# Performance work log

Measured on AMD Instinct MI355X. Metric: run time of the kernel, lower is better.

## Reference

```python
import jax, jax.numpy as jnp
import numpy as np

NEG_SLOPE = 0.2  # PyG GATConv default LeakyReLU slope


def _gat(h, src, dst, num_nodes, W, a_src, a_dst, bias):
    """PyG-style GATConv (concat=True, eval mode, self-loops already in src/dst)."""
    heads, out = a_src.shape
    hp = (h @ W).reshape(num_nodes, heads, out)          # (N, H, F)
    e_s = (hp * a_src).sum(-1)                            # (N, H)
    e_d = (hp * a_dst).sum(-1)                            # (N, H)
    e = jax.nn.leaky_relu(e_s[src] + e_d[dst], NEG_SLOPE)  # (E, H)
    m = jax.ops.segment_max(e, dst, num_segments=num_nodes)
    w = jnp.exp(e - m[dst])
    z = jax.ops.segment_sum(w, dst, num_segments=num_nodes)
    alpha = w / (z[dst] + 1e-16)                          # softmax over in-edges per dst
    agg = jax.ops.segment_sum(hp[src] * alpha[:, :, None], dst, num_segments=num_nodes)
    return agg.reshape(num_nodes, heads * out) + bias


def setup_inputs() -> dict:
    key = jax.random.key(0)
    ks = jax.random.split(key, 20)
    N, T, Fin, H, heads, E = 30000, 4, 256, 64, 4, 240000
    D = H * heads  # 256
    s = 0.05
    p = lambda k, shape: (jax.random.normal(k, shape, jnp.float32) * s)
    return {
        "x": jax.random.normal(ks[0], (N, T, Fin), jnp.float32),
        "edge_index": jax.random.randint(ks[1], (2, E), 0, N, jnp.int32),
        "Wp": p(ks[2], (Fin, H)), "bp": p(ks[3], (H,)),
        "W0": p(ks[4], (H, D)), "a_src0": p(ks[5], (heads, H)), "a_dst0": p(ks[6], (heads, H)), "b0": p(ks[7], (D,)),
        "W1": p(ks[8], (D, D)), "a_src1": p(ks[9], (heads, H)), "a_dst1": p(ks[10], (heads, H)), "b1": p(ks[11], (D,)),
        "Wq": p(ks[12], (D, D)), "bq": p(ks[13], (D,)),
        "Wk": p(ks[14], (D, D)), "bk": p(ks[15], (D,)),
        "Wv": p(ks[16], (D, D)), "bv": p(ks[17], (D,)),
    }


def reference(x, edge_index, Wp, bp, W0, a_src0, a_dst0, b0, W1, a_src1, a_dst1, b1,
              Wq, bq, Wk, bk, Wv, bv):
    N, T, Fin = x.shape
    D = Wq.shape[0]
    loops = jnp.arange(N, dtype=edge_index.dtype)
    src = jnp.concatenate([edge_index[0], loops])  # add self-loops (PyG default)
    dst = jnp.concatenate([edge_index[1], loops])
    xT = jnp.transpose(x, (1, 0, 2))  # (T, N, Fin)

    def step(_, xt):
        h = xt @ Wp + bp
        h = jax.nn.elu(_gat(h, src, dst, N, W0, a_src0, a_dst0, b0))
        h = jax.nn.elu(_gat(h, src, dst, N, W1, a_src1, a_dst1, b1))
        return None, h

    _, embs = jax.lax.scan(step, None, xT)  # (T, N, D)

    # temporal attention
    Q = embs @ Wq + bq
    K = embs @ Wk + bk
    V = embs @ Wv + bv
    Q_time = Q.mean(axis=1)  # (T, D)
    K_time = K.mean(axis=1)  # (T, D)
    scores = (Q_time @ K_time.T) / jnp.sqrt(jnp.asarray(D, jnp.float32))
    attn = jax.nn.softmax(scores, axis=1)            # (T, T)
    Vr = V.reshape(T, -1)                            # (T, N*D)
    attended = attn @ Vr                             # (T, N*D)
    return attended[-1].reshape(N, D)
```

## Files before the change

### kernel.cpp

```cpp
#include <hip/hip_runtime.h>
#include <math.h>

#define NEG_SLOPE 0.2f

typedef __attribute__((ext_vector_type(8))) short short8;
typedef __attribute__((ext_vector_type(4))) float f32x4;

__device__ inline unsigned short f2bf(float f){
  union { float f; unsigned u; } v; v.f = f;
  unsigned r = v.u + 0x7fffu + ((v.u >> 16) & 1u);
  return (unsigned short)(r >> 16);
}
__device__ inline float bf2f(unsigned u){
  union { unsigned u; float f; } v; v.u = u << 16; return v.f;
}

__global__ __launch_bounds__(256) void k_deg_count(const int* __restrict__ dst, int E, int* __restrict__ deg){
  int i = blockIdx.x*256 + threadIdx.x;
  if (i < E) atomicAdd(&deg[dst[i]], 1);
}
__global__ __launch_bounds__(256) void k_scan_blk(const int* __restrict__ deg, int* __restrict__ rowptr,
                                                  int* __restrict__ bsum, int N){
  __shared__ int ws[4];
  int tid = threadIdx.x;
  int i = blockIdx.x*256 + tid;
  int v = (i < N) ? deg[i]+1 : 0;
  int lane = tid & 63, w = tid >> 6;
  int s = v;
  #pragma unroll
  for (int off=1; off<64; off<<=1){
    int u = __shfl_up(s, off);
    if (lane >= off) s += u;
  }
  if (lane == 63) ws[w] = s;
  __syncthreads();
  int woff = 0;
  #pragma unroll
  for (int k=0;k<4;k++) if (k < w) woff += ws[k];
  int incl = s + woff;
  if (i < N) rowptr[i] = incl - v;
  if (tid == 255) bsum[blockIdx.x] = incl;
}
__global__ __launch_bounds__(256) void k_scan_top(int* __restrict__ bsum, int nb, int* __restrict__ rowptrN){
  __shared__ int buf[256];
  int tid = threadIdx.x;
  int v = (tid < nb) ? bsum[tid] : 0;
  buf[tid] = v;
  __syncthreads();
  for (int off=1; off<256; off<<=1){
    int add = (tid >= off) ? buf[tid-off] : 0;
    __syncthreads();
    buf[tid] += add;
    __syncthreads();
  }
  if (tid < nb) bsum[tid] = buf[tid] - v;
  if (tid == 0) rowptrN[0] = buf[255];
}
__global__ __launch_bounds__(256) void k_scan_fix(int* __restrict__ rowptr, const int* __restrict__ bsum,
                                                  int* __restrict__ pos, int* __restrict__ colidx, int N){
  int i = blockIdx.x*256 + threadIdx.x;
  if (i < N){
    int r = rowptr[i] + bsum[blockIdx.x];
    rowptr[i] = r;
    colidx[r] = i;
    pos[i] = r + 1;
  }
}
__global__ __launch_bounds__(256) void k_fill_edges(const int* __restrict__ src, const int* __restrict__ dst,
                                                    int E, int* __restrict__ pos, int* __restrict__ colidx){
  int i = blockIdx.x*256 + threadIdx.x;
  if (i < E){
    int d = dst[i];
    colidx[atomicAdd(&pos[d],1)] = src[i];
  }
}

__global__ __launch_bounds__(256) void k_prep(const float* __restrict__ Wp, const float* __restrict__ W0,
                                              const float* __restrict__ W1, const float* __restrict__ Wv,
                                              const float* __restrict__ as0, const float* __restrict__ ad0,
                                              unsigned short* __restrict__ WpT, unsigned short* __restrict__ W0T4,
                                              unsigned short* __restrict__ W1T, unsigned short* __restrict__ WvT,
                                              float* __restrict__ ahs, float* __restrict__ ahd,
                                              int* __restrict__ deg, float* __restrict__ sume, int N){
  int idx = blockIdx.x*256 + threadIdx.x;
  if (idx < 16384){
    int k = idx >> 6, p = idx & 63;
    WpT[p*256 + k] = f2bf(Wp[idx]);
  } else if (idx < 32768){
    int i = idx - 16384;
    int h = i >> 12, r = i & 4095, p = r >> 6, k = r & 63;
    W0T4[i] = f2bf(W0[k*256 + h*64 + p]);
  } else if (idx < 98304){
    int i = idx - 32768; int k = i >> 8, p = i & 255;
    W1T[p*256 + k] = f2bf(W1[i]);
  } else if (idx < 163840){
    int i = idx - 98304; int k = i >> 8, p = i & 255;
    WvT[p*256 + k] = f2bf(Wv[i]);
  } else if (idx < 164096){
    int i = idx - 163840;
    int h = i >> 6, d = i & 63;
    float ss = 0.f, sd = 0.f;
    for (int j=0;j<64;j++){
      float w = W0[d*256 + h*64 + j];
      ss += w * as0[h*64 + j];
      sd += w * ad0[h*64 + j];
    }
    ahs[i] = ss; ahd[i] = sd;
  } else if (idx < 165120){
    sume[idx - 164096] = 0.f;
  } else if (idx < 165120 + N){
    deg[idx - 165120] = 0;
  }
}

__global__ __launch_bounds__(256) void k_h0(const float* __restrict__ A,
                                            const unsigned short* __restrict__ Bt,
                                            const float* __restrict__ bias,
                                            unsigned short* __restrict__ C, int M, int Nn){
  int wid = blockIdx.x*4 + (threadIdx.x >> 6);
  int m0 = wid * 64;
  if (m0 >= M) return;
  int lane = threadIdx.x & 63;
  int lr = lane & 15, g = lane >> 4, lk = g*8;
  const float* Arow[4];
  #pragma unroll
  for (int m=0;m<4;m++){
    int row = m0 + m*16 + lr;
    if (row > M-1) row = M-1;
    Arow[m] = A + (size_t)row*256 + lk;
  }
  const unsigned short* Bb = Bt + (size_t)lr*256 + lk;
  f32x4 acc[4][4];
  #pragma unroll
  for (int m=0;m<4;m++)
    #pragma unroll
    for (int n=0;n<4;n++)
      #pragma unroll
      for (int j=0;j<4;j++) acc[m][n][j] = 0.f;

  #pragma unroll 2
  for (int ks=0; ks<8; ks++){
    int k0 = ks*32;
    short8 bfr[4];
    #pragma unroll
    for (int n=0;n<4;n++)
      bfr[n] = *(const short8*)(Bb + (size_t)n*16*256 + k0);
    short8 afr[4];
    #pragma unroll
    for (int m=0;m<4;m++){
      float4 u = *(const float4*)(Arow[m] + k0);
      float4 w = *(const float4*)(Arow[m] + k0 + 4);
      afr[m][0]=(short)f2bf(u.x); afr[m][1]=(short)f2bf(u.y);
      afr[m][2]=(short)f2bf(u.z); afr[m][3]=(short)f2bf(u.w);
      afr[m][4]=(short)f2bf(w.x); afr[m][5]=(short)f2bf(w.y);
      afr[m][6]=(short)f2bf(w.z); afr[m][7]=(short)f2bf(w.w);
    }
    #pragma unroll
    for (int m=0;m<4;m++)
      #pragma unroll
      for (int n=0;n<4;n++)
        acc[m][n] = __builtin_amdgcn_mfma_f32_16x16x32_bf16(afr[m], bfr[n], acc[m][n], 0,0,0);
  }
  #pragma unroll
  for (int n=0;n<4;n++){
    int col = n*16 + lr;
    float bcol = bias[col];
    #pragma unroll
    for (int m=0;m<4;m++){
      #pragma unroll
      for (int j=0;j<4;j++){
        int row = m0 + m*16 + g*4 + j;
        if (row < M){
          int t = row & 3, nn = row >> 2;
          C[(size_t)t*Nn*64 + (size_t)nn*64 + col] = f2bf(acc[m][n][j] + bcol);
        }
      }
    }
  }
}

__global__ __launch_bounds__(256) void k_gat01(const unsigned short* __restrict__ A,
                                               const unsigned short* __restrict__ W0T4,
                                               const float* __restrict__ b0,
                                               const unsigned short* __restrict__ W1T,
                                               const float* __restrict__ as1,
                                               const float* __restrict__ ad1,
                                               unsigned short* __restrict__ hp,
                                               float* __restrict__ e_s, float* __restrict__ e_d,
                                               int M){
  __shared__ unsigned short H1[64][264];
  __shared__ unsigned short Bls[128][72];
  int tid = threadIdx.x;
  int m0 = blockIdx.x * 64;
  int wave = tid >> 6, lane = tid & 63;
  int lr = lane & 15, g4 = lane >> 4, lk = g4*8;
  int rbase = m0 + wave*16;

  {
    f32x4 acc1[16];
    #pragma unroll
    for (int q=0;q<16;q++)
      #pragma unroll
      for (int j=0;j<4;j++) acc1[q][j] = 0.f;
    int arow = rbase + lr; if (arow > M-1) arow = M-1;
    #pragma unroll
    for (int h=0;h<4;h++){
      short8 afr[2];
      #pragma unroll
      for (int ks=0;ks<2;ks++)
        afr[ks] = *(const short8*)(A + (size_t)arow*256 + h*64 + ks*32 + lk);
      #pragma unroll
      for (int nn=0;nn<4;nn++){
        #pragma unroll
        for (int ks=0;ks<2;ks++){
          short8 bfr = *(const short8*)(W0T4 + ((size_t)h*64 + nn*16 + lr)*64 + ks*32 + lk);
          acc1[h*4+nn] = __builtin_amdgcn_mfma_f32_16x16x32_bf16(afr[ks], bfr, acc1[h*4+nn], 0,0,0);
        }
      }
    }
    #pragma unroll
    for (int q=0;q<16;q++){
      int col = q*16 + lr;
      float bcol = b0[col];
      #pragma unroll
      for (int j=0;j<4;j++){
        float v = acc1[q][j] + bcol;
        v = (v > 0.f) ? v : (__expf(v) - 1.f);
        H1[wave*16 + g4*4 + j][col] = f2bf(v);
      }
    }
  }
  __syncthreads();

  float esp0[4], esp1[4], esp2[4], esp3[4];
  float edp0[4], edp1[4], edp2[4], edp3[4];
  #pragma unroll
  for (int j=0;j<4;j++){ esp0[j]=0.f; esp1[j]=0.f; esp2[j]=0.f; esp3[j]=0.f;
                         edp0[j]=0.f; edp1[j]=0.f; edp2[j]=0.f; edp3[j]=0.f; }

  #pragma unroll
  for (int chalf=0; chalf<2; chalf++){
    f32x4 acc2[8];
    #pragma unroll
    for (int q=0;q<8;q++)
      #pragma unroll
      for (int j=0;j<4;j++) acc2[q][j] = 0.f;
    for (int k0=0;k0<256;k0+=64){
      #pragma unroll
      for (int it=0; it<4; it++){
        int idx = tid + it*256;
        int p = idx >> 3, ch = (idx & 7)*8;
        *(uint4*)(&Bls[p][ch]) = *(const uint4*)(W1T + (size_t)(chalf*128 + p)*256 + k0 + ch);
      }
      __syncthreads();
      #pragma unroll
      for (int ks=0;ks<2;ks++){
        short8 afr = *(const short8*)(&H1[wave*16 + lr][k0 + ks*32 + lk]);
        #pragma unroll
        for (int q=0;q<8;q++){
          short8 bfr = *(const short8*)(&Bls[q*16 + lr][ks*32 + lk]);
          acc2[q] = __builtin_amdgcn_mfma_f32_16x16x32_bf16(afr, bfr, acc2[q], 0,0,0);
        }
      }
      __syncthreads();
    }
    #pragma unroll
    for (int q=0;q<8;q++){
      int col = chalf*128 + q*16 + lr;
      float asv = as1[col], adv = ad1[col];
      #pragma unroll
      for (int j=0;j<4;j++){
        int row = m0 + wave*16 + g4*4 + j;
        float v = acc2[q][j];
        if (row < M)
          hp[(size_t)row*256 + col] = f2bf(v);
        if (chalf==0 && (q>>2)==0){ esp0[j] += v*asv; edp0[j] += v*adv; }
        if (chalf==0 && (q>>2)==1){ esp1[j] += v*asv; edp1[j] += v*adv; }
        if (chalf==1 && (q>>2)==0){ esp2[j] += v*asv; edp2[j] += v*adv; }
        if (chalf==1 && (q>>2)==1){ esp3[j] += v*asv; edp3[j] += v*adv; }
      }
    }
  }

  #pragma unroll
  for (int j=0;j<4;j++){
    #pragma unroll
    for (int off=1; off<16; off<<=1){
      esp0[j] += __shfl_xor(esp0[j], off); edp0[j] += __shfl_xor(edp0[j], off);
      esp1[j] += __shfl_xor(esp1[j], off); edp1[j] += __shfl_xor(edp1[j], off);
      esp2[j] += __shfl_xor(esp2[j], off); edp2[j] += __shfl_xor(edp2[j], off);
      esp3[j] += __shfl_xor(esp3[j], off); edp3[j] += __shfl_xor(edp3[j], off);
    }
  }
  if (lr < 4){
    #pragma unroll
    for (int j=0;j<4;j++){
      int row = m0 + wave*16 + g4*4 + j;
      if (row < M){
        float ev = (lr==0)?esp0[j]:((lr==1)?esp1[j]:((lr==2)?esp2[j]:esp3[j]));
        float dv = (lr==0)?edp0[j]:((lr==1)?edp1[j]:((lr==2)?edp2[j]:edp3[j]));
        e_s[(size_t)row*4 + lr] = ev;
        e_d[(size_t)row*4 + lr] = dv;
      }
    }
  }
}

__global__ __launch_bounds__(512) void k_gemm_fin(const unsigned short* __restrict__ embs,
                                                  const float* __restrict__ awp,
                                                  const unsigned short* __restrict__ Bt,
                                                  const float* __restrict__ bias,
                                                  float* __restrict__ C, int M){
  constexpr int K = 256, BK = 64, PAD = 8;
  __shared__ unsigned short Als[128][BK+PAD];
  __shared__ unsigned short Bls[256][BK+PAD];
  int tid = threadIdx.x;
  int m0  = blockIdx.x * 128;
  int wave = tid >> 6, lane = tid & 63;
  int wr = wave & 3, wc = wave >> 2;
  int lr = lane & 15, lk = (lane >> 4) * 8;
  float a0=awp[0], a1=awp[1], a2=awp[2], a3=awp[3];
  size_t sl = (size_t)M*256;
  f32x4 acc[2][8];
  #pragma unroll
  for (int m=0;m<2;m++)
    #pragma unroll
    for (int n=0;n<8;n++)
      #pragma unroll
      for (int j=0;j<4;j++) acc[m][n][j] = 0.f;

  for (int k0 = 0; k0 < K; k0 += BK){
    #pragma unroll
    for (int i=0;i<2;i++){
      int idx = tid + i*512;
      int r = idx >> 3, ch = (idx & 7)*8;
      int row = m0 + r;
      uint4 w = make_uint4(0,0,0,0);
      if (row < M){
        size_t o = (size_t)row*256 + k0 + ch;
        uint4 u0 = *(const uint4*)(embs + o);
        uint4 u1 = *(const uint4*)(embs + o + sl);
        uint4 u2 = *(const uint4*)(embs + o + 2*sl);
        uint4 u3 = *(const uint4*)(embs + o + 3*sl);
        const unsigned* p0=&u0.x; const unsigned* p1=&u1.x;
        const unsigned* p2=&u2.x; const unsigned* p3=&u3.x;
        unsigned* pw=&w.x;
        #pragma unroll
        for (int q=0;q<4;q++){
          float lo = a0*bf2f(p0[q]&0xffffu) + a1*bf2f(p1[q]&0xffffu) + a2*bf2f(p2[q]&0xffffu) + a3*bf2f(p3[q]&0xffffu);
          float hi = a0*bf2f(p0[q]>>16)     + a1*bf2f(p1[q]>>16)     + a2*bf2f(p2[q]>>16)     + a3*bf2f(p3[q]>>16);
          pw[q] = (unsigned)f2bf(lo) | ((unsigned)f2bf(hi) << 16);
        }
      }
      *(uint4*)(&Als[r][ch]) = w;
    }
    #pragma unroll
    for (int i=0;i<4;i++){
      int idx = tid + i*512;
      int r = idx >> 3, ch = (idx & 7)*8;
      *(uint4*)(&Bls[r][ch]) = *(const uint4*)(Bt + (size_t)r*K + k0 + ch);
    }
    __syncthreads();
    #pragma unroll
    for (int ks=0; ks<2; ks++){
      short8 afr[2], bfr[8];
      #pragma unroll
      for (int m=0;m<2;m++)
        afr[m] = *(const short8*)(&Als[wr*32 + m*16 + lr][ks*32 + lk]);
      #pragma unroll
      for (int n=0;n<8;n++)
        bfr[n] = *(const short8*)(&Bls[wc*128 + n*16 + lr][ks*32 + lk]);
      #pragma unroll
      for (int m=0;m<2;m++)
        #pragma unroll
        for (int n=0;n<8;n++)
          acc[m][n] = __builtin_amdgcn_mfma_f32_16x16x32_bf16(afr[m], bfr[n], acc[m][n], 0,0,0);
    }
    __syncthreads();
  }
  #pragma unroll
  for (int m=0;m<2;m++){
    #pragma unroll
    for (int n=0;n<8;n++){
      int col = wc*128 + n*16 + lr;
      float bcol = bias[col];
      #pragma unroll
      for (int j=0;j<4;j++){
        int row = m0 + wr*32 + m*16 + (lane>>4)*4 + j;
        if (row < M)
          C[(size_t)row*256 + col] = acc[m][n][j] + bcol;
      }
    }
  }
}

__global__ __launch_bounds__(256) void k_esd0(const unsigned short* __restrict__ h0,
                                              const float* __restrict__ ahs, const float* __restrict__ ahd,
                                              float* __restrict__ e_s, float* __restrict__ e_d, int M){
  int n = blockIdx.x*4 + (threadIdx.x >> 6);
  if (n >= M) return;
  int lane = threadIdx.x & 63;
  int h = lane >> 4, l4 = (lane & 15)*4;
  uint2 v = *(const uint2*)(h0 + (size_t)n*64 + l4);
  float v0 = bf2f(v.x & 0xffffu), v1 = bf2f(v.x >> 16);
  float v2 = bf2f(v.y & 0xffffu), v3 = bf2f(v.y >> 16);
  float4 as = *(const float4*)(ahs + h*64 + l4);
  float4 ad = *(const float4*)(ahd + h*64 + l4);
  float ps = v0*as.x + v1*as.y + v2*as.z + v3*as.w;
  float pd = v0*ad.x + v1*ad.y + v2*ad.z + v3*ad.w;
  #pragma unroll
  for (int off=1; off<16; off<<=1){ ps += __shfl_xor(ps,off); pd += __shfl_xor(pd,off); }
  if ((lane & 15) == 0){
    e_s[n*4+h] = ps; e_d[n*4+h] = pd;
  }
}

__global__ __launch_bounds__(256) void k_agg0(const unsigned short* __restrict__ h0all,
                                              const float* __restrict__ e_s, const float* __restrict__ e_d,
                                              const int* __restrict__ rowptr, const int* __restrict__ colidx,
                                              unsigned short* __restrict__ agg, int N){
  int n = blockIdx.x*4 + (threadIdx.x >> 6);
  if (n >= N) return;
  int t = blockIdx.y;
  int g = t*N + n;
  int lane = threadIdx.x & 63;
  int half = lane >> 5, l = lane & 31;
  int h = l >> 3, di = (l & 7)*8;
  int s0 = rowptr[n], s1 = rowptr[n+1];
  float ed = e_d[(size_t)g*4 + h];
  const unsigned short* h0t = h0all + (size_t)t*N*64;
  const float* est = e_s + (size_t)t*N*4;
  float z = 0.f;
  float a[8] = {0,0,0,0,0,0,0,0};
  int i = s0;
  for (; i+6 <= s1; i += 6){
    int sA = colidx[i + half];
    int sB = colidx[i + 2 + half];
    int sC = colidx[i + 4 + half];
    uint4 vA = *(const uint4*)(h0t + (size_t)sA*64 + di);
    uint4 vB = *(const uint4*)(h0t + (size_t)sB*64 + di);
    uint4 vC = *(const uint4*)(h0t + (size_t)sC*64 + di);
    float eA = est[sA*4 + h] + ed;
    float eB = est[sB*4 + h] + ed;
    float eC = est[sC*4 + h] + ed;
    eA = fmaxf(eA, NEG_SLOPE*eA); eB = fmaxf(eB, NEG_SLOPE*eB); eC = fmaxf(eC, NEG_SLOPE*eC);
    float wA = __expf(eA), wB = __expf(eB), wC = __expf(eC);
    z += wA + wB + wC;
    a[0] += wA*bf2f(vA.x&0xffffu) + wB*bf2f(vB.x&0xffffu) + wC*bf2f(vC.x&0xffffu);
    a[1] += wA*bf2f(vA.x>>16)     + wB*bf2f(vB.x>>16)     + wC*bf2f(vC.x>>16);
    a[2] += wA*bf2f(vA.y&0xffffu) + wB*bf2f(vB.y&0xffffu) + wC*bf2f(vC.y&0xffffu);
    a[3] += wA*bf2f(vA.y>>16)     + wB*bf2f(vB.y>>16)     + wC*bf2f(vC.y>>16);
    a[4] += wA*bf2f(vA.z&0xffffu) + wB*bf2f(vB.z&0xffffu) + wC*bf2f(vC.z&0xffffu);
    a[5] += wA*bf2f(vA.z>>16)     + wB*bf2f(vB.z>>16)     + wC*bf2f(vC.z>>16);
    a[6] += wA*bf2f(vA.w&0xffffu) + wB*bf2f(vB.w&0xffffu) + wC*bf2f(vC.w&0xffffu);
    a[7] += wA*bf2f(vA.w>>16)     + wB*bf2f(vB.w>>16)     + wC*bf2f(vC.w>>16);
  }
  for (; i+2 <= s1; i += 2){
    int s = colidx[i + half];
    uint4 v = *(const uint4*)(h0t + (size_t)s*64 + di);
    float e = est[s*4 + h] + ed;
    e = fmaxf(e, NEG_SLOPE*e);
    float w = __expf(e);
    z += w;
    a[0] += w*bf2f(v.x&0xffffu); a[1] += w*bf2f(v.x>>16);
    a[2] += w*bf2f(v.y&0xffffu); a[3] += w*bf2f(v.y>>16);
    a[4] += w*bf2f(v.z&0xffffu); a[5] += w*bf2f(v.z>>16);
    a[6] += w*bf2f(v.w&0xffffu); a[7] += w*bf2f(v.w>>16);
  }
  if (i < s1 && half == 0){
    int s = colidx[i];
    uint4 v = *(const uint4*)(h0t + (size_t)s*64 + di);
    float e = est[s*4 + h] + ed;
    e = fmaxf(e, NEG_SLOPE*e);
    float w = __expf(e);
    z += w;
    a[0] += w*bf2f(v.x&0xffffu); a[1] += w*bf2f(v.x>>16);
    a[2] += w*bf2f(v.y&0xffffu); a[3] += w*bf2f(v.y>>16);
    a[4] += w*bf2f(v.z&0xffffu); a[5] += w*bf2f(v.z>>16);
    a[6] += w*bf2f(v.w&0xffffu); a[7] += w*bf2f(v.w>>16);
  }
  z += __shfl_xor(z, 32);
  #pragma unroll
  for (int q=0;q<8;q++) a[q] += __shfl_xor(a[q], 32);
  if (half == 0){
    float inv = 1.f / (z + 1e-16f);
    uint4 r;
    r.x = (unsigned)f2bf(a[0]*inv) | ((unsigned)f2bf(a[1]*inv) << 16);
    r.y = (unsigned)f2bf(a[2]*inv) | ((unsigned)f2bf(a[3]*inv) << 16);
    r.z = (unsigned)f2bf(a[4]*inv) | ((unsigned)f2bf(a[5]*inv) << 16);
    r.w = (unsigned)f2bf(a[6]*inv) | ((unsigned)f2bf(a[7]*inv) << 16);
    *(uint4*)(agg + (size_t)g*256 + l*8) = r;
  }
}

__global__ __launch_bounds__(256) void k_agg(const unsigned short* __restrict__ hpall,
                                             const float* __restrict__ e_s, const float* __restrict__ e_d,
                                             const int* __restrict__ rowptr, const int* __restrict__ colidx,
                                             const float* __restrict__ bias, unsigned short* __restrict__ outb,
                                             int N){
  int n = blockIdx.x*4 + (threadIdx.x >> 6);
  if (n >= N) return;
  int t = blockIdx.y;
  int g = t*N + n;
  int lane = threadIdx.x & 63;
  int half = lane >> 5, l = lane & 31;
  int h = l >> 3, d0 = l*8;
  int s0 = rowptr[n], s1 = rowptr[n+1];
  float ed = e_d[(size_t)g*4 + h];
  const unsigned short* hpt = hpall + (size_t)t*N*256;
  const float* est = e_s + (size_t)t*N*4;
  float z = 0.f;
  float a[8] = {0,0,0,0,0,0,0,0};
  int i = s0;
  for (; i+6 <= s1; i += 6){
    int sA = colidx[i + half];
    int sB = colidx[i + 2 + half];
    int sC = colidx[i + 4 + half];
    uint4 vA = *(const uint4*)(hpt + (size_t)sA*256 + d0);
    uint4 vB = *(const uint4*)(hpt + (size_t)sB*256 + d0);
    uint4 vC = *(const uint4*)(hpt + (size_t)sC*256 + d0);
    float eA = est[sA*4 + h] + ed;
    float eB = est[sB*4 + h] + ed;
    float eC = est[sC*4 + h] + ed;
    eA = fmaxf(eA, NEG_SLOPE*eA); eB = fmaxf(eB, NEG_SLOPE*eB); eC = fmaxf(eC, NEG_SLOPE*eC);
    float wA = __expf(eA), wB = __expf(eB), wC = __expf(eC);
    z += wA + wB + wC;
    a[0] += wA*bf2f(vA.x&0xffffu) + wB*bf2f(vB.x&0xffffu) + wC*bf2f(vC.x&0xffffu);
    a[1] += wA*bf2f(vA.x>>16)     + wB*bf2f(vB.x>>16)     + wC*bf2f(vC.x>>16);
    a[2] += wA*bf2f(vA.y&0xffffu) + wB*bf2f(vB.y&0xffffu) + wC*bf2f(vC.y&0xffffu);
    a[3] += wA*bf2f(vA.y>>16)     + wB*bf2f(vB.y>>16)     + wC*bf2f(vC.y>>16);
    a[4] += wA*bf2f(vA.z&0xffffu) + wB*bf2f(vB.z&0xffffu) + wC*bf2f(vC.z&0xffffu);
    a[5] += wA*bf2f(vA.z>>16)     + wB*bf2f(vB.z>>16)     + wC*bf2f(vC.z>>16);
    a[6] += wA*bf2f(vA.w&0xffffu) + wB*bf2f(vB.w&0xffffu) + wC*bf2f(vC.w&0xffffu);
    a[7] += wA*bf2f(vA.w>>16)     + wB*bf2f(vB.w>>16)     + wC*bf2f(vC.w>>16);
  }
  for (; i+2 <= s1; i += 2){
    int s = colidx[i + half];
    uint4 v = *(const uint4*)(hpt + (size_t)s*256 + d0);
    float e = est[s*4 + h] + ed;
    e = fmaxf(e, NEG_SLOPE*e);
    float w = __expf(e);
    z += w;
    a[0] += w*bf2f(v.x&0xffffu); a[1] += w*bf2f(v.x>>16);
    a[2] += w*bf2f(v.y&0xffffu); a[3] += w*bf2f(v.y>>16);
    a[4] += w*bf2f(v.z&0xffffu); a[5] += w*bf2f(v.z>>16);
    a[6] += w*bf2f(v.w&0xffffu); a[7] += w*bf2f(v.w>>16);
  }
  if (i < s1 && half == 0){
    int s = colidx[i];
    uint4 v = *(const uint4*)(hpt + (size_t)s*256 + d0);
    float e = est[s*4 + h] + ed;
    e = fmaxf(e, NEG_SLOPE*e);
    float w = __expf(e);
    z += w;
    a[0] += w*bf2f(v.x&0xffffu); a[1] += w*bf2f(v.x>>16);
    a[2] += w*bf2f(v.y&0xffffu); a[3] += w*bf2f(v.y>>16);
    a[4] += w*bf2f(v.z&0xffffu); a[5] += w*bf2f(v.z>>16);
    a[6] += w*bf2f(v.w&0xffffu); a[7] += w*bf2f(v.w>>16);
  }
  z += __shfl_xor(z, 32);
  #pragma unroll
  for (int q=0;q<8;q++) a[q] += __shfl_xor(a[q], 32);
  if (half == 0){
    float inv = 1.f / (z + 1e-16f);
    float4 bA = *(const float4*)(bias + d0);
    float4 bB = *(const float4*)(bias + d0 + 4);
    float o[8];
    o[0]=a[0]*inv+bA.x; o[1]=a[1]*inv+bA.y; o[2]=a[2]*inv+bA.z; o[3]=a[3]*inv+bA.w;
    o[4]=a[4]*inv+bB.x; o[5]=a[5]*inv+bB.y; o[6]=a[6]*inv+bB.z; o[7]=a[7]*inv+bB.w;
    #pragma unroll
    for (int q=0;q<8;q++) o[q] = (o[q] > 0.f) ? o[q] : (__expf(o[q]) - 1.f);
    uint4 r;
    r.x = (unsigned)f2bf(o[0]) | ((unsigned)f2bf(o[1]) << 16);
    r.y = (unsigned)f2bf(o[2]) | ((unsigned)f2bf(o[3]) << 16);
    r.z = (unsigned)f2bf(o[4]) | ((unsigned)f2bf(o[5]) << 16);
    r.w = (unsigned)f2bf(o[6]) | ((unsigned)f2bf(o[7]) << 16);
    *(uint4*)(outb + (size_t)g*256 + d0) = r;
  }
}

__global__ __launch_bounds__(256) void k_colsum(const unsigned short* __restrict__ emb, float* __restrict__ sums, int N){
  __shared__ float red[8][256];
  int tid = threadIdx.x;
  int t = blockIdx.x >> 6, chunk = blockIdx.x & 63;
  int rows_per = (N + 63) / 64;
  int r0 = chunk * rows_per;
  int r1 = min(N, r0 + rows_per);
  const unsigned short* base = emb + (size_t)t*N*256;
  int c0 = (tid & 31)*8, rg = tid >> 5;
  float s[8] = {0,0,0,0,0,0,0,0};
  for (int r = r0 + rg; r < r1; r += 8){
    uint4 v = *(const uint4*)(base + (size_t)r*256 + c0);
    s[0] += bf2f(v.x & 0xffffu); s[1] += bf2f(v.x >> 16);
    s[2] += bf2f(v.y & 0xffffu); s[3] += bf2f(v.y >> 16);
    s[4] += bf2f(v.z & 0xffffu); s[5] += bf2f(v.z >> 16);
    s[6] += bf2f(v.w & 0xffffu); s[7] += bf2f(v.w >> 16);
  }
  #pragma unroll
  for (int j=0;j<8;j++) red[rg][c0+j] = s[j];
  __syncthreads();
  float tot = 0.f;
  #pragma unroll
  for (int g=0;g<8;g++) tot += red[g][tid];
  atomicAdd(&sums[t*256 + tid], tot);
}

__global__ __launch_bounds__(256) void k_attn(const float* __restrict__ sum_emb,
                                              const float* __restrict__ Wq, const float* __restrict__ bq,
                                              const float* __restrict__ Wk, const float* __restrict__ bk,
                                              float* __restrict__ aw, int N){
  __shared__ float mean_s[4][256];
  __shared__ float red[256];
  __shared__ float scores_s[4];
  int j = threadIdx.x;
  float invN = 1.0f/(float)N;
  #pragma unroll
  for (int t=0;t<4;t++) mean_s[t][j] = sum_emb[t*256+j]*invN;
  __syncthreads();
  float q3 = bq[j];
  float kt0=bk[j], kt1=bk[j], kt2=bk[j], kt3=bk[j];
  for (int m=0;m<256;m++){
    float wq = Wq[m*256+j];
    float wk = Wk[m*256+j];
    float m0 = mean_s[0][m], m1 = mean_s[1][m], m2 = mean_s[2][m], m3 = mean_s[3][m];
    q3  += m3*wq;
    kt0 += m0*wk; kt1 += m1*wk; kt2 += m2*wk; kt3 += m3*wk;
  }
  float kts0=kt0, kts1=kt1, kts2=kt2, kts3=kt3;
  #pragma unroll
  for (int t=0;t<4;t++){
    float ktv = (t==0)?kts0:((t==1)?kts1:((t==2)?kts2:kts3));
    red[j] = q3*ktv;
    __syncthreads();
    for (int off=128; off>0; off>>=1){
      if (j < off) red[j] += red[j+off];
      __syncthreads();
    }
    if (j==0) scores_s[t] = red[0]*(1.0f/16.0f);
    __syncthreads();
  }
  if (j==0){
    float mx = fmaxf(fmaxf(scores_s[0],scores_s[1]),fmaxf(scores_s[2],scores_s[3]));
    float w0 = __expf(scores_s[0]-mx), w1 = __expf(scores_s[1]-mx),
          w2 = __expf(scores_s[2]-mx), w3 = __expf(scores_s[3]-mx);
    float s = w0+w1+w2+w3;
    aw[0]=w0/s; aw[1]=w1/s; aw[2]=w2/s; aw[3]=w3/s;
  }
}

extern "C" void kernel_launch(void* const* d_in, const int* in_sizes, int n_in,
                              void* d_out, int out_size, void* d_ws, size_t ws_size,
                              hipStream_t stream){
  (void)n_in; (void)out_size; (void)ws_size;
  const float* x   = (const float*)d_in[0];
  const int*   ei  = (const int*)d_in[1];
  const float* Wp  = (const float*)d_in[2];
  const float* bp  = (const float*)d_in[3];
  const float* W0  = (const float*)d_in[4];
  const float* as0 = (const float*)d_in[5];
  const float* ad0 = (const float*)d_in[6];
  const float* b0  = (const float*)d_in[7];
  const float* W1  = (const float*)d_in[8];
  const float* as1 = (const float*)d_in[9];
  const float* ad1 = (const float*)d_in[10];
  const float* b1  = (const float*)d_in[11];
  const float* Wq  = (const float*)d_in[12];
  const float* bq  = (const float*)d_in[13];
  const float* Wk  = (const float*)d_in[14];
  const float* bk  = (const float*)d_in[15];
  const float* Wv  = (const float*)d_in[16];
  const float* bv  = (const float*)d_in[17];
  float* out = (float*)d_out;

  const int T = 4, FIN = 256;
  const int N = in_sizes[0] / (T*FIN);
  const int E = in_sizes[1] / 2;
  const int TN = T*N;
  const int* src = ei;
  const int* dst = ei + E;

  char* ws = (char*)d_ws;
  size_t cur = 0;
  auto alloc = [&](size_t bytes)->void*{
    void* p = ws + cur;
    cur += (bytes + 255) & ~(size_t)255;
    return p;
  };
  unsigned short* h0all = (unsigned short*)alloc((size_t)TN*64*2);
  unsigned short* bufA  = (unsigned short*)alloc((size_t)TN*256*2);
  unsigned short* bufB  = (unsigned short*)alloc((size_t)TN*256*2);
  unsigned short* embs  = (unsigned short*)alloc((size_t)TN*256*2);
  float* e_s    = (float*)alloc((size_t)TN*4*4);
  float* e_d    = (float*)alloc((size_t)TN*4*4);
  float* sume   = (float*)alloc(4*256*4);
  float* aw     = (float*)alloc(256);
  float* ah0s   = (float*)alloc(256*4);
  float* ah0d   = (float*)alloc(256*4);
  int*   rowptr = (int*)alloc((size_t)(N+1)*4);
  int*   deg    = (int*)alloc((size_t)N*4);
  int*   pos    = (int*)alloc((size_t)N*4);
  int*   bsum   = (int*)alloc((size_t)256*4);
  int*   colidx = (int*)alloc((size_t)(E+N)*4);
  unsigned short* WpT  = (unsigned short*)alloc((size_t)64*256*2);
  unsigned short* W0T4 = (unsigned short*)alloc((size_t)4*64*64*2);
  unsigned short* W1T  = (unsigned short*)alloc((size_t)256*256*2);
  unsigned short* WvT  = (unsigned short*)alloc((size_t)256*256*2);

  int nb256 = (N+255)/256;
  int nbE   = (E+255)/256;
  int gmN   = (N+127)/128;
  int gagg  = (TN+3)/4;

  int prep_total = 165120 + N;
  k_prep<<<(prep_total+255)/256,256,0,stream>>>(Wp, W0, W1, Wv, as0, ad0,
                                                WpT, W0T4, W1T, WvT, ah0s, ah0d, deg, sume, N);

  k_deg_count<<<nbE,256,0,stream>>>(dst, E, deg);
  k_scan_blk<<<nb256,256,0,stream>>>(deg, rowptr, bsum, N);
  k_scan_top<<<1,256,0,stream>>>(bsum, nb256, rowptr + N);
  k_scan_fix<<<nb256,256,0,stream>>>(rowptr, bsum, pos, colidx, N);
  k_fill_edges<<<nbE,256,0,stream>>>(src, dst, E, pos, colidx);

  k_h0<<<(TN/64+3)/4 + 1,256,0,stream>>>(x, WpT, bp, h0all, TN, N);

  k_esd0<<<gagg,256,0,stream>>>(h0all, ah0s, ah0d, e_s, e_d, TN);
  k_agg0<<<dim3((N+3)/4, T),256,0,stream>>>(h0all, e_s, e_d, rowptr, colidx, bufA, N);
  k_gat01<<<(TN+63)/64,256,0,stream>>>(bufA, W0T4, b0, W1T, as1, ad1, bufB, e_s, e_d, TN);
  k_agg<<<dim3((N+3)/4, T),256,0,stream>>>(bufB, e_s, e_d, rowptr, colidx, b1, embs, N);
  k_colsum<<<256,256,0,stream>>>(embs, sume, N);

  k_attn<<<1,256,0,stream>>>(sume, Wq, bq, Wk, bk, aw, N);
  k_gemm_fin<<<gmN,512,0,stream>>>(embs, aw, WvT, bv, out, N);
}
```

Before: 405.9 us.

## Split fused GAT0/GAT1 GEMM kernel into per-head GEMM plus tiled 128x256 GEMM

Replaces the fused k_gat01 kernel, which computed the layer-0 per-head projection into shared memory and then the layer-1 GEMM, with two kernels. k_gat0 computes the per-head bf16 GEMM plus bias and ELU and writes it to a new global buffer. k_gemm_hp does a 128x256 LDS-tiled MFMA GEMM that also emits the attention logits e_s/e_d. This gives the second GEMM better B-tile reuse across 128 rows and more waves per block. In exchange the intermediate activations take an extra global write and read round trip, plus one more launch.

```diff
diff --git a/kernel.cpp b/kernel.cpp
--- a/kernel.cpp
+++ b/kernel.cpp
@@ -179,128 +179,168 @@
   }
 }
 
-__global__ __launch_bounds__(256) void k_gat01(const unsigned short* __restrict__ A,
-                                               const unsigned short* __restrict__ W0T4,
-                                               const float* __restrict__ b0,
-                                               const unsigned short* __restrict__ W1T,
-                                               const float* __restrict__ as1,
-                                               const float* __restrict__ ad1,
-                                               unsigned short* __restrict__ hp,
-                                               float* __restrict__ e_s, float* __restrict__ e_d,
-                                               int M){
-  __shared__ unsigned short H1[64][264];
-  __shared__ unsigned short Bls[128][72];
-  int tid = threadIdx.x;
-  int m0 = blockIdx.x * 64;
-  int wave = tid >> 6, lane = tid & 63;
-  int lr = lane & 15, g4 = lane >> 4, lk = g4*8;
-  int rbase = m0 + wave*16;
-
-  {
-    f32x4 acc1[16];
-    #pragma unroll
-    for (int q=0;q<16;q++)
-      #pragma unroll
-      for (int j=0;j<4;j++) acc1[q][j] = 0.f;
-    int arow = rbase + lr; if (arow > M-1) arow = M-1;
-    #pragma unroll
-    for (int h=0;h<4;h++){
-      short8 afr[2];
-      #pragma unroll
-      for (int ks=0;ks<2;ks++)
-        afr[ks] = *(const short8*)(A + (size_t)arow*256 + h*64 + ks*32 + lk);
-      #pragma unroll
-      for (int nn=0;nn<4;nn++){
-        #pragma unroll
-        for (int ks=0;ks<2;ks++){
-          short8 bfr = *(const short8*)(W0T4 + ((size_t)h*64 + nn*16 + lr)*64 + ks*32 + lk);
-          acc1[h*4+nn] = __builtin_amdgcn_mfma_f32_16x16x32_bf16(afr[ks], bfr, acc1[h*4+nn], 0,0,0);
+__global__ __launch_bounds__(256) void k_gat0(const unsigned short* __restrict__ A,
+                                              const unsigned short* __restrict__ W0T4,
+                                              const float* __restrict__ b0,
+                                              unsigned short* __restrict__ C, int M){
+  int h = blockIdx.y;
+  int wid = blockIdx.x*4 + (threadIdx.x >> 6);
+  int m0 = wid * 64;
+  if (m0 >= M) return;
+  int lane = threadIdx.x & 63;
+  int lr = lane & 15, g = lane >> 4, lk = g*8;
+  const unsigned short* Wh = W0T4 + (size_t)h*64*64;
+  f32x4 acc[4][4];
+  #pragma unroll
+  for (int m=0;m<4;m++)
+    #pragma unroll
+    for (int n=0;n<4;n++)
+      #pragma unroll
+      for (int j=0;j<4;j++) acc[m][n][j] = 0.f;
+
+  #pragma unroll
+  for (int ks=0; ks<2; ks++){
+    short8 bfr[4], afr[4];
+    #pragma unroll
+    for (int n=0;n<4;n++)
+      bfr[n] = *(const short8*)(Wh + (size_t)(n*16+lr)*64 + ks*32 + lk);
+    #pragma unroll
+    for (int m=0;m<4;m++){
+      int row = m0 + m*16 + lr;
+      if (row > M-1) row = M-1;
+      afr[m] = *(const short8*)(A + (size_t)row*256 + h*64 + ks*32 + lk);
+    }
+    #pragma unroll
+    for (int m=0;m<4;m++)
+      #pragma unroll
+      for (int n=0;n<4;n++)
+        acc[m][n] = __builtin_amdgcn_mfma_f32_16x16x32_bf16(afr[m], bfr[n], acc[m][n], 0,0,0);
+  }
+  #pragma unroll
+  for (int n=0;n<4;n++){
+    int col = h*64 + n*16 + lr;
+    float bcol = b0[col];
+    #pragma unroll
+    for (int m=0;m<4;m++){
+      #pragma unroll
+      for (int j=0;j<4;j++){
+        int row = m0 + m*16 + g*4 + j;
+        if (row < M){
+          float v = acc[m][n][j] + bcol;
+          v = (v > 0.f) ? v : (__expf(v) - 1.f);
+          C[(size_t)row*256 + col] = f2bf(v);
         }
       }
     }
-    #pragma unroll
-    for (int q=0;q<16;q++){
-      int col = q*16 + lr;
-      float bcol = b0[col];
+  }
+}
+
+__global__ __launch_bounds__(512) void k_gemm_hp(const unsigned short* __restrict__ A,
+                                                 const unsigned short* __restrict__ Bt,
+                                                 const float* __restrict__ as1,
+                                                 const float* __restrict__ ad1,
+                                                 unsigned short* __restrict__ hp,
+                                                 float* __restrict__ e_s, float* __restrict__ e_d,
+                                                 int M){
+  constexpr int K = 256, BK = 64, PAD = 8;
+  __shared__ unsigned short Als[128][BK+PAD];
+  __shared__ unsigned short Bls[256][BK+PAD];
+  int tid = threadIdx.x;
+  int m0  = blockIdx.x * 128;
+  int wave = tid >> 6, lane = tid & 63;
+  int wr = wave & 3, wc = wave >> 2;
+  int lr = lane & 15, g4 = lane >> 4, lk = g4*8;
+  f32x4 acc[2][8];
+  #pragma unroll
+  for (int m=0;m<2;m++)
+    #pragma unroll
+    for (int n=0;n<8;n++)
+      #pragma unroll
+      for (int j=0;j<4;j++) acc[m][n][j] = 0.f;
+
+  for (int k0 = 0; k0 < K; k0 += BK){
+    #pragma unroll
+    for (int i=0;i<2;i++){
+      int idx = tid + i*512;
+      int r = idx >> 3, ch = (idx & 7)*8;
+      int row = m0 + r;
+      uint4 v = make_uint4(0,0,0,0);
+      if (row < M) v = *(const uint4*)(A + (size_t)row*256 + k0 + ch);
+      *(uint4*)(&Als[r][ch]) = v;
+    }
+    #pragma unroll
+    for (int i=0;i<4;i++){
+      int idx = tid + i*512;
+      int r = idx >> 3, ch = (idx & 7)*8;
+      *(uint4*)(&Bls[r][ch]) = *(const uint4*)(Bt + (size_t)r*K + k0 + ch);
+    }
+    __syncthreads();
+    #pragma unroll
+    for (int ks=0; ks<2; ks++){
+      short8 afr[2], bfr[8];
+      #pragma unroll
+      for (int m=0;m<2;m++)
+        afr[m] = *(const short8*)(&Als[wr*32 + m*16 + lr][ks*32 + lk]);
+      #pragma unroll
+      for (int n=0;n<8;n++)
+        bfr[n] = *(const short8*)(&Bls[wc*128 + n*16 + lr][ks*32 + lk]);
+      #pragma unroll
+      for (int m=0;m<2;m++)
+        #pragma unroll
+        for (int n=0;n<8;n++)
+          acc[m][n] = __builtin_amdgcn_mfma_f32_16x16x32_bf16(afr[m], bfr[n], acc[m][n], 0,0,0);
+    }
+    __syncthreads();
+  }
+
+  float esA[2][4], esB[2][4], edA[2][4], edB[2][4];
+  #pragma unroll
+  for (int m=0;m<2;m++)
+    #pragma unroll
+    for (int j=0;j<4;j++){ esA[m][j]=0.f; esB[m][j]=0.f; edA[m][j]=0.f; edB[m][j]=0.f; }
+
+  #pragma unroll
+  for (int m=0;m<2;m++){
+    #pragma unroll
+    for (int n=0;n<8;n++){
+      int col = wc*128 + n*16 + lr;
+      float asv = as1[col], adv = ad1[col];
       #pragma unroll
       for (int j=0;j<4;j++){
-        float v = acc1[q][j] + bcol;
-        v = (v > 0.f) ? v : (__expf(v) - 1.f);
-        H1[wave*16 + g4*4 + j][col] = f2bf(v);
-      }
-    }
-  }
-  __syncthreads();
-
-  float esp0[4], esp1[4], esp2[4], esp3[4];
-  float edp0[4], edp1[4], edp2[4], edp3[4];
-  #pragma unroll
-  for (int j=0;j<4;j++){ esp0[j]=0.f; esp1[j]=0.f; esp2[j]=0.f; esp3[j]=0.f;
-                         edp0[j]=0.f; edp1[j]=0.f; edp2[j]=0.f; edp3[j]=0.f; }
-
-  #pragma unroll
-  for (int chalf=0; chalf<2; chalf++){
-    f32x4 acc2[8];
-    #pragma unroll
-    for (int q=0;q<8;q++)
-      #pragma unroll
-      for (int j=0;j<4;j++) acc2[q][j] = 0.f;
-    for (int k0=0;k0<256;k0+=64){
-      #pragma unroll
-      for (int it=0; it<4; it++){
-        int idx = tid + it*256;
-        int p = idx >> 3, ch = (idx & 7)*8;
-        *(uint4*)(&Bls[p][ch]) = *(const uint4*)(W1T + (size_t)(chalf*128 + p)*256 + k0 + ch);
-      }
-      __syncthreads();
-      #pragma unroll
-      for (int ks=0;ks<2;ks++){
-        short8 afr = *(const short8*)(&H1[wave*16 + lr][k0 + ks*32 + lk]);
-        #pragma unroll
-        for (int q=0;q<8;q++){
-          short8 bfr = *(const short8*)(&Bls[q*16 + lr][ks*32 + lk]);
-          acc2[q] = __builtin_amdgcn_mfma_f32_16x16x32_bf16(afr, bfr, acc2[q], 0,0,0);
-        }
-      }
-      __syncthreads();
-    }
-    #pragma unroll
-    for (int q=0;q<8;q++){
-      int col = chalf*128 + q*16 + lr;
-      float asv = as1[col], adv = ad1[col];
-      #pragma unroll
-      for (int j=0;j<4;j++){
-        int row = m0 + wave*16 + g4*4 + j;
-        float v = acc2[q][j];
+        int row = m0 + wr*32 + m*16 + g4*4 + j;
+        float v = acc[m][n][j];
         if (row < M)
           hp[(size_t)row*256 + col] = f2bf(v);
-        if (chalf==0 && (q>>2)==0){ esp0[j] += v*asv; edp0[j] += v*adv; }
-        if (chalf==0 && (q>>2)==1){ esp1[j] += v*asv; edp1[j] += v*adv; }
-        if (chalf==1 && (q>>2)==0){ esp2[j] += v*asv; edp2[j] += v*adv; }
-        if (chalf==1 && (q>>2)==1){ esp3[j] += v*asv; edp3[j] += v*adv; }
+        if (n < 4){ esA[m][j] += v*asv; edA[m][j] += v*adv; }
+        else      { esB[m][j] += v*asv; edB[m][j] += v*adv; }
       }
     }
   }
-
-  #pragma unroll
-  for (int j=0;j<4;j++){
-    #pragma unroll
-    for (int off=1; off<16; off<<=1){
-      esp0[j] += __shfl_xor(esp0[j], off); edp0[j] += __shfl_xor(edp0[j], off);
-      esp1[j] += __shfl_xor(esp1[j], off); edp1[j] += __shfl_xor(edp1[j], off);
-      esp2[j] += __shfl_xor(esp2[j], off); edp2[j] += __shfl_xor(edp2[j], off);
-      esp3[j] += __shfl_xor(esp3[j], off); edp3[j] += __shfl_xor(edp3[j], off);
-    }
-  }
-  if (lr < 4){
+  #pragma unroll
+  for (int m=0;m<2;m++){
     #pragma unroll
     for (int j=0;j<4;j++){
-      int row = m0 + wave*16 + g4*4 + j;
-      if (row < M){
-        float ev = (lr==0)?esp0[j]:((lr==1)?esp1[j]:((lr==2)?esp2[j]:esp3[j]));
-        float dv = (lr==0)?edp0[j]:((lr==1)?edp1[j]:((lr==2)?edp2[j]:edp3[j]));
-        e_s[(size_t)row*4 + lr] = ev;
-        e_d[(size_t)row*4 + lr] = dv;
+      #pragma unroll
+      for (int off=1; off<16; off<<=1){
+        esA[m][j] += __shfl_xor(esA[m][j], off);
+        esB[m][j] += __shfl_xor(esB[m][j], off);
+        edA[m][j] += __shfl_xor(edA[m][j], off);
+        edB[m][j] += __shfl_xor(edB[m][j], off);
+      }
+    }
+  }
+  if (lr == 0){
+    #pragma unroll
+    for (int m=0;m<2;m++){
+      #pragma unroll
+      for (int j=0;j<4;j++){
+        int row = m0 + wr*32 + m*16 + g4*4 + j;
+        if (row < M){
+          e_s[(size_t)row*4 + 2*wc]     = esA[m][j];
+          e_s[(size_t)row*4 + 2*wc + 1] = esB[m][j];
+          e_d[(size_t)row*4 + 2*wc]     = edA[m][j];
+          e_d[(size_t)row*4 + 2*wc + 1] = edB[m][j];
+        }
       }
     }
   }
@@ -689,6 +729,7 @@
   unsigned short* h0all = (unsigned short*)alloc((size_t)TN*64*2);
   unsigned short* bufA  = (unsigned short*)alloc((size_t)TN*256*2);
   unsigned short* bufB  = (unsigned short*)alloc((size_t)TN*256*2);
+  unsigned short* bufC  = (unsigned short*)alloc((size_t)TN*256*2);
   unsigned short* embs  = (unsigned short*)alloc((size_t)TN*256*2);
   float* e_s    = (float*)alloc((size_t)TN*4*4);
   float* e_d    = (float*)alloc((size_t)TN*4*4);
@@ -709,6 +750,7 @@
   int nb256 = (N+255)/256;
   int nbE   = (E+255)/256;
   int gmN   = (N+127)/128;
+  int gmTN  = (TN+127)/128;
   int gagg  = (TN+3)/4;
 
   int prep_total = 165120 + N;
@@ -725,8 +767,9 @@
 
   k_esd0<<<gagg,256,0,stream>>>(h0all, ah0s, ah0d, e_s, e_d, TN);
   k_agg0<<<dim3((N+3)/4, T),256,0,stream>>>(h0all, e_s, e_d, rowptr, colidx, bufA, N);
-  k_gat01<<<(TN+63)/64,256,0,stream>>>(bufA, W0T4, b0, W1T, as1, ad1, bufB, e_s, e_d, TN);
-  k_agg<<<dim3((N+3)/4, T),256,0,stream>>>(bufB, e_s, e_d, rowptr, colidx, b1, embs, N);
+  k_gat0<<<dim3((TN+255)/256, 4),256,0,stream>>>(bufA, W0T4, b0, bufB, TN);
+  k_gemm_hp<<<gmTN,512,0,stream>>>(bufB, W1T, as1, ad1, bufC, e_s, e_d, TN);
+  k_agg<<<dim3((N+3)/4, T),256,0,stream>>>(bufC, e_s, e_d, rowptr, colidx, b1, embs, N);
   k_colsum<<<256,256,0,stream>>>(embs, sume, N);
 
   k_attn<<<1,256,0,stream>>>(sume, Wq, bq, Wk, bk, aw, N);
```

Measured after the change: 432.4 us. 1.07x slower.
